# Performance work log

Hardware: AMD Instinct MI355X
Metric: run time of the kernel (lower is better)

The kernel has to match this reference:

```python
import jax, jax.numpy as jnp
import numpy as np

EMBED_DIM = 256
NUM_HEADS = 8
WINDOW = 64
HEAD_DIM = EMBED_DIM // NUM_HEADS


def setup_inputs() -> dict:
    key = jax.random.key(0)
    k_x, k_w, k_ow = jax.random.split(key, 3)
    B, S, E = 2, 4096, EMBED_DIM
    x = jax.random.normal(k_x, (B, S, E), dtype=jnp.float32)
    # nn.MultiheadAttention params: packed in_proj (q,k,v) and out_proj
    bound = 1.0 / np.sqrt(E)
    in_proj_w = jax.random.uniform(k_w, (3 * E, E), jnp.float32, -bound, bound)
    in_proj_b = jnp.zeros((3 * E,), jnp.float32)
    out_w = jax.random.uniform(k_ow, (E, E), jnp.float32, -bound, bound)
    out_b = jnp.zeros((E,), jnp.float32)
    return {"x": x, "in_proj_w": in_proj_w, "in_proj_b": in_proj_b,
            "out_w": out_w, "out_b": out_b}


def reference(x, in_proj_w, in_proj_b, out_w, out_b):
    B, S, E = x.shape
    H, D = NUM_HEADS, HEAD_DIM
    # packed qkv projection (torch Linear: y = x @ W^T + b)
    qkv = jnp.einsum('bse,fe->bsf', x, in_proj_w) + in_proj_b  # [B,S,3E]
    q, k, v = jnp.split(qkv, 3, axis=-1)
    q = q.reshape(B, S, H, D).transpose(0, 2, 1, 3)  # [B,H,S,D]
    k = k.reshape(B, S, H, D).transpose(0, 2, 1, 3)
    v = v.reshape(B, S, H, D).transpose(0, 2, 1, 3)
    scale = 1.0 / jnp.sqrt(jnp.asarray(D, x.dtype))
    scores = jnp.einsum('bhqd,bhkd->bhqk', q * scale, k)  # [B,H,S,S]
    idx = jnp.arange(S)
    band = jnp.abs(idx[:, None] - idx[None, :]) <= WINDOW  # [S,S]
    neg = jnp.asarray(-1e9, scores.dtype)
    scores = jnp.where(band[None, None, :, :], scores, neg)
    attn = jax.nn.softmax(scores, axis=-1)
    out = jnp.einsum('bhqk,bhkd->bhqd', attn, v)  # [B,H,S,D]
    out = out.transpose(0, 2, 1, 3).reshape(B, S, E)
    return jnp.einsum('bse,fe->bsf', out, out_w) + out_b
```

## Files before the change

### kernel.cpp

```cpp
#include <hip/hip_runtime.h>
#include <hip/hip_bf16.h>

#define S_LEN 4096
#define EMB   256
#define NHEAD 8
#define HDIM  32
#define WIN   64
#define BATCH 2

typedef __attribute__((ext_vector_type(8))) short short8;
typedef __attribute__((ext_vector_type(4))) float floatx4;

static __device__ __forceinline__ unsigned int bf16_rn(float x) {
    unsigned int u = __float_as_uint(x);
    return (u + 0x7FFFu + ((u >> 16) & 1u)) >> 16;
}
static __device__ __forceinline__ void split2(float x, unsigned int& hi, unsigned int& lo) {
    hi = bf16_rn(x);
    const float hf = __uint_as_float(hi << 16);
    lo = bf16_rn(x - hf);
}
static __device__ __forceinline__ void split_store4(unsigned short* hp, unsigned short* lp, float4 v) {
    unsigned int h0, l0, h1, l1, h2, l2, h3, l3;
    split2(v.x, h0, l0); split2(v.y, h1, l1);
    split2(v.z, h2, l2); split2(v.w, h3, l3);
    uint2 hv, lv;
    hv.x = h0 | (h1 << 16); hv.y = h2 | (h3 << 16);
    lv.x = l0 | (l1 << 16); lv.y = l2 | (l3 << 16);
    *(uint2*)hp = hv;
    *(uint2*)lp = lv;
}

#define LDA 40

__global__ __launch_bounds__(256) void qkv_proj_kernel(
    const float* __restrict__ X, const float* __restrict__ W,
    const float* __restrict__ bias,
    float* __restrict__ Qb, float* __restrict__ Kb, float* __restrict__ Vb)
{
    __shared__ __align__(16) unsigned short Ah[128 * LDA], Al[128 * LDA];
    __shared__ __align__(16) unsigned short Bh[64 * LDA],  Bl[64 * LDA];
    const int tid = threadIdx.x;
    const int m0 = blockIdx.y * 128, n0 = blockIdx.x * 64;
    const int r0 = tid >> 3, c4 = tid & 7;
    const int lane = tid & 63, wv = tid >> 6;
    const int wm = (wv >> 1) * 64, wn = (wv & 1) * 32;
    const int lm = lane & 15, kq = lane >> 4;

    float4 ar[4], wr[2];
#pragma unroll
    for (int r = 0; r < 4; ++r)
        ar[r] = *(const float4*)(X + (size_t)(m0 + r0 + r * 32) * EMB + c4 * 4);
#pragma unroll
    for (int r = 0; r < 2; ++r)
        wr[r] = *(const float4*)(W + (size_t)(n0 + r0 + r * 32) * EMB + c4 * 4);

    floatx4 acc[4][2] = {};
    for (int t = 0; t < 8; ++t) {
        __syncthreads();
#pragma unroll
        for (int r = 0; r < 4; ++r)
            split_store4(&Ah[(r0 + r * 32) * LDA + c4 * 4], &Al[(r0 + r * 32) * LDA + c4 * 4], ar[r]);
#pragma unroll
        for (int r = 0; r < 2; ++r)
            split_store4(&Bh[(r0 + r * 32) * LDA + c4 * 4], &Bl[(r0 + r * 32) * LDA + c4 * 4], wr[r]);
        __syncthreads();
        if (t < 7) {
            const int k0 = (t + 1) * 32;
#pragma unroll
            for (int r = 0; r < 4; ++r)
                ar[r] = *(const float4*)(X + (size_t)(m0 + r0 + r * 32) * EMB + k0 + c4 * 4);
#pragma unroll
            for (int r = 0; r < 2; ++r)
                wr[r] = *(const float4*)(W + (size_t)(n0 + r0 + r * 32) * EMB + k0 + c4 * 4);
        }
        short8 a_h[4], a_l[4], b_h[2], b_l[2];
#pragma unroll
        for (int mt = 0; mt < 4; ++mt) {
            a_h[mt] = *(const short8*)&Ah[(wm + mt * 16 + lm) * LDA + kq * 8];
            a_l[mt] = *(const short8*)&Al[(wm + mt * 16 + lm) * LDA + kq * 8];
        }
#pragma unroll
        for (int nt = 0; nt < 2; ++nt) {
            b_h[nt] = *(const short8*)&Bh[(wn + nt * 16 + lm) * LDA + kq * 8];
            b_l[nt] = *(const short8*)&Bl[(wn + nt * 16 + lm) * LDA + kq * 8];
        }
#pragma unroll
        for (int mt = 0; mt < 4; ++mt)
#pragma unroll
            for (int nt = 0; nt < 2; ++nt) {
                acc[mt][nt] = __builtin_amdgcn_mfma_f32_16x16x32_bf16(a_h[mt], b_h[nt], acc[mt][nt], 0, 0, 0);
                acc[mt][nt] = __builtin_amdgcn_mfma_f32_16x16x32_bf16(a_h[mt], b_l[nt], acc[mt][nt], 0, 0, 0);
                acc[mt][nt] = __builtin_amdgcn_mfma_f32_16x16x32_bf16(a_l[mt], b_h[nt], acc[mt][nt], 0, 0, 0);
            }
    }
#pragma unroll
    for (int nt = 0; nt < 2; ++nt) {
        const int f = n0 + wn + nt * 16 + lm;
        const int which = f >> 8;
        const int h = (f & 255) >> 5, d = f & 31;
        float* dst = (which == 0) ? Qb : ((which == 1) ? Kb : Vb);
        const float sc = (which == 0) ? 0.17677669529663687f : 1.0f;
        const float bf = bias[f];
#pragma unroll
        for (int mt = 0; mt < 4; ++mt)
#pragma unroll
            for (int r = 0; r < 4; ++r) {
                const int m = m0 + wm + mt * 16 + kq * 4 + r;
                const int b = m >> 12, s = m & (S_LEN - 1);
                dst[(((size_t)b * NHEAD + h) * S_LEN + s) * HDIM + d] = (acc[mt][nt][r] + bf) * sc;
            }
    }
}

__global__ __launch_bounds__(256) void out_proj_kernel(
    const float* __restrict__ A, const float* __restrict__ W,
    const float* __restrict__ bias, float* __restrict__ C)
{
    __shared__ __align__(16) unsigned short Ah[128 * LDA], Al[128 * LDA];
    __shared__ __align__(16) unsigned short Bh[64 * LDA],  Bl[64 * LDA];
    const int tid = threadIdx.x;
    const int m0 = blockIdx.y * 128, n0 = blockIdx.x * 64;
    const int r0 = tid >> 3, c4 = tid & 7;
    const int lane = tid & 63, wv = tid >> 6;
    const int wm = (wv >> 1) * 64, wn = (wv & 1) * 32;
    const int lm = lane & 15, kq = lane >> 4;

    float4 ar[4], wr[2];
#pragma unroll
    for (int r = 0; r < 4; ++r)
        ar[r] = *(const float4*)(A + (size_t)(m0 + r0 + r * 32) * EMB + c4 * 4);
#pragma unroll
    for (int r = 0; r < 2; ++r)
        wr[r] = *(const float4*)(W + (size_t)(n0 + r0 + r * 32) * EMB + c4 * 4);

    floatx4 acc[4][2] = {};
    for (int t = 0; t < 8; ++t) {
        __syncthreads();
#pragma unroll
        for (int r = 0; r < 4; ++r)
            split_store4(&Ah[(r0 + r * 32) * LDA + c4 * 4], &Al[(r0 + r * 32) * LDA + c4 * 4], ar[r]);
#pragma unroll
        for (int r = 0; r < 2; ++r)
            split_store4(&Bh[(r0 + r * 32) * LDA + c4 * 4], &Bl[(r0 + r * 32) * LDA + c4 * 4], wr[r]);
        __syncthreads();
        if (t < 7) {
            const int k0 = (t + 1) * 32;
#pragma unroll
            for (int r = 0; r < 4; ++r)
                ar[r] = *(const float4*)(A + (size_t)(m0 + r0 + r * 32) * EMB + k0 + c4 * 4);
#pragma unroll
            for (int r = 0; r < 2; ++r)
                wr[r] = *(const float4*)(W + (size_t)(n0 + r0 + r * 32) * EMB + k0 + c4 * 4);
        }
        short8 a_h[4], a_l[4], b_h[2], b_l[2];
#pragma unroll
        for (int mt = 0; mt < 4; ++mt) {
            a_h[mt] = *(const short8*)&Ah[(wm + mt * 16 + lm) * LDA + kq * 8];
            a_l[mt] = *(const short8*)&Al[(wm + mt * 16 + lm) * LDA + kq * 8];
        }
#pragma unroll
        for (int nt = 0; nt < 2; ++nt) {
            b_h[nt] = *(const short8*)&Bh[(wn + nt * 16 + lm) * LDA + kq * 8];
            b_l[nt] = *(const short8*)&Bl[(wn + nt * 16 + lm) * LDA + kq * 8];
        }
#pragma unroll
        for (int mt = 0; mt < 4; ++mt)
#pragma unroll
            for (int nt = 0; nt < 2; ++nt) {
                acc[mt][nt] = __builtin_amdgcn_mfma_f32_16x16x32_bf16(a_h[mt], b_h[nt], acc[mt][nt], 0, 0, 0);
                acc[mt][nt] = __builtin_amdgcn_mfma_f32_16x16x32_bf16(a_h[mt], b_l[nt], acc[mt][nt], 0, 0, 0);
                acc[mt][nt] = __builtin_amdgcn_mfma_f32_16x16x32_bf16(a_l[mt], b_h[nt], acc[mt][nt], 0, 0, 0);
            }
    }
#pragma unroll
    for (int nt = 0; nt < 2; ++nt) {
        const int f = n0 + wn + nt * 16 + lm;
        const float bf = bias[f];
#pragma unroll
        for (int mt = 0; mt < 4; ++mt)
#pragma unroll
            for (int r = 0; r < 4; ++r) {
                const int m = m0 + wm + mt * 16 + kq * 4 + r;
                C[(size_t)m * EMB + f] = acc[mt][nt][r] + bf;
            }
    }
}

#define AKS 40
#define AVS 200
#define APS 200

__global__ __launch_bounds__(256) void local_attn_kernel(
    const float* __restrict__ Qb, const float* __restrict__ Kb,
    const float* __restrict__ Vb, float* __restrict__ Ab)
{
    __shared__ __align__(16) unsigned short Qh[64 * AKS], Ql[64 * AKS];
    __shared__ __align__(16) unsigned short Kh[192 * AKS], Kl[192 * AKS];
    __shared__ __align__(16) unsigned short Vt[32 * AVS];
    __shared__ __align__(16) unsigned short Pw[4 * 16 * APS];

    const int tid = threadIdx.x;
    const int q0 = blockIdx.x * 64;
    const int h = blockIdx.y, b = blockIdx.z;
    const int jmin = max(0, q0 - WIN);
    const int jmax = min(S_LEN - 1, q0 + 63 + WIN);
    const int nk = jmax - jmin + 1;
    const size_t bhS = ((size_t)b * NHEAD + h) * S_LEN;
    const float* Qg = Qb + (bhS + q0) * HDIM;
    const float* Kg = Kb + (bhS + jmin) * HDIM;
    const float* Vg = Vb + (bhS + jmin) * HDIM;

    const int r0 = tid >> 3, c4 = tid & 7;
#pragma unroll
    for (int r = 0; r < 2; ++r) {
        const int row = r0 + r * 32;
        const float4 v = *(const float4*)&Qg[row * HDIM + c4 * 4];
        split_store4(&Qh[row * AKS + c4 * 4], &Ql[row * AKS + c4 * 4], v);
    }
#pragma unroll
    for (int r = 0; r < 6; ++r) {
        const int t = r0 + r * 32;
        const int tc = min(t, nk - 1);
        const float4 v = *(const float4*)&Kg[tc * HDIM + c4 * 4];
        split_store4(&Kh[t * AKS + c4 * 4], &Kl[t * AKS + c4 * 4], v);
    }
#pragma unroll
    for (int r = 0; r < 6; ++r) {
        const int t = r0 + r * 32;
        const int tc = min(t, nk - 1);
        const float4 v = *(const float4*)&Vg[tc * HDIM + c4 * 4];
        Vt[(c4 * 4 + 0) * AVS + t] = (unsigned short)bf16_rn(v.x);
        Vt[(c4 * 4 + 1) * AVS + t] = (unsigned short)bf16_rn(v.y);
        Vt[(c4 * 4 + 2) * AVS + t] = (unsigned short)bf16_rn(v.z);
        Vt[(c4 * 4 + 3) * AVS + t] = (unsigned short)bf16_rn(v.w);
    }
    __syncthreads();

    const int lane = tid & 63, wv = tid >> 6;
    const int lm = lane & 15, quad = lane >> 4;
    const int qbase = wv * 16;

    const short8 qh = *(const short8*)&Qh[(qbase + lm) * AKS + quad * 8];
    const short8 ql = *(const short8*)&Ql[(qbase + lm) * AKS + quad * 8];

    floatx4 sacc[12];
#pragma unroll
    for (int nt = 0; nt < 12; ++nt) {
        const short8 bh = *(const short8*)&Kh[(nt * 16 + lm) * AKS + quad * 8];
        const short8 bl = *(const short8*)&Kl[(nt * 16 + lm) * AKS + quad * 8];
        floatx4 a = {};
        a = __builtin_amdgcn_mfma_f32_16x16x32_bf16(qh, bh, a, 0, 0, 0);
        a = __builtin_amdgcn_mfma_f32_16x16x32_bf16(qh, bl, a, 0, 0, 0);
        a = __builtin_amdgcn_mfma_f32_16x16x32_bf16(ql, bh, a, 0, 0, 0);
        sacc[nt] = a;
    }

    const int qg = q0 + qbase + quad * 4;
    float mx[4] = {-1e30f, -1e30f, -1e30f, -1e30f};
#pragma unroll
    for (int nt = 0; nt < 12; ++nt) {
        const int slot = nt * 16 + lm;
        const int keyg = jmin + slot;
#pragma unroll
        for (int r = 0; r < 4; ++r) {
            const int qr = qg + r;
            const bool valid = (slot < nk) && (keyg >= qr - WIN) && (keyg <= qr + WIN);
            const float sv = valid ? sacc[nt][r] : -1e30f;
            sacc[nt][r] = sv;
            mx[r] = fmaxf(mx[r], sv);
        }
    }
#pragma unroll
    for (int r = 0; r < 4; ++r) {
        mx[r] = fmaxf(mx[r], __shfl_xor(mx[r], 1));
        mx[r] = fmaxf(mx[r], __shfl_xor(mx[r], 2));
        mx[r] = fmaxf(mx[r], __shfl_xor(mx[r], 4));
        mx[r] = fmaxf(mx[r], __shfl_xor(mx[r], 8));
    }
    float l[4] = {0.f, 0.f, 0.f, 0.f};
    unsigned short* Pme = &Pw[wv * 16 * APS];
#pragma unroll
    for (int nt = 0; nt < 12; ++nt)
#pragma unroll
        for (int r = 0; r < 4; ++r) {
            const float p = __expf(sacc[nt][r] - mx[r]);
            l[r] += p;
            Pme[(quad * 4 + r) * APS + nt * 16 + lm] = (unsigned short)bf16_rn(p);
        }
#pragma unroll
    for (int r = 0; r < 4; ++r) {
        l[r] += __shfl_xor(l[r], 1);
        l[r] += __shfl_xor(l[r], 2);
        l[r] += __shfl_xor(l[r], 4);
        l[r] += __shfl_xor(l[r], 8);
    }
    const float rl[4] = {1.f / l[0], 1.f / l[1], 1.f / l[2], 1.f / l[3]};

    floatx4 oacc[2] = {};
#pragma unroll
    for (int ks = 0; ks < 6; ++ks) {
        const short8 ap  = *(const short8*)&Pme[lm * APS + ks * 32 + quad * 8];
        const short8 bv0 = *(const short8*)&Vt[lm * AVS + ks * 32 + quad * 8];
        const short8 bv1 = *(const short8*)&Vt[(16 + lm) * AVS + ks * 32 + quad * 8];
        oacc[0] = __builtin_amdgcn_mfma_f32_16x16x32_bf16(ap, bv0, oacc[0], 0, 0, 0);
        oacc[1] = __builtin_amdgcn_mfma_f32_16x16x32_bf16(ap, bv1, oacc[1], 0, 0, 0);
    }
#pragma unroll
    for (int nt = 0; nt < 2; ++nt)
#pragma unroll
        for (int r = 0; r < 4; ++r) {
            const int qrow = qbase + quad * 4 + r;
            Ab[((size_t)b * S_LEN + q0 + qrow) * EMB + h * HDIM + nt * 16 + lm]
                = oacc[nt][r] * rl[r];
        }
}

extern "C" void kernel_launch(void* const* d_in, const int* in_sizes, int n_in,
                              void* d_out, int out_size, void* d_ws, size_t ws_size,
                              hipStream_t stream) {
    const float* x  = (const float*)d_in[0];
    const float* wi = (const float*)d_in[1];
    const float* bi = (const float*)d_in[2];
    const float* wo = (const float*)d_in[3];
    const float* bo = (const float*)d_in[4];
    float* out = (float*)d_out;

    const size_t per = (size_t)BATCH * NHEAD * S_LEN * HDIM;
    float* Qb = (float*)d_ws;
    float* Kb = Qb + per;
    float* Vb = Kb + per;
    float* Ab = Vb + per;

    qkv_proj_kernel<<<dim3(768 / 64, 8192 / 128), 256, 0, stream>>>(x, wi, bi, Qb, Kb, Vb);
    local_attn_kernel<<<dim3(S_LEN / 64, NHEAD, BATCH), 256, 0, stream>>>(Qb, Kb, Vb, Ab);
    out_proj_kernel<<<dim3(256 / 64, 8192 / 128), 256, 0, stream>>>(Ab, wo, bo, out);
}
```

Baseline: 117.0 us.

## Pre-split inputs into bf16 hi/lo once and pass bf16 intermediates between kernels

Adds a conversion kernel that splits X and both weight matrices into bf16 hi/lo planes once, instead of every GEMM block re-splitting fp32 tiles. Q/K/V and the attention output are now stored as bf16 hi/lo (V as a single bf16), so the GEMM and attention kernels load pre-split data with straight 16-byte copies into shared memory. This removes redundant split arithmetic across the 12 column blocks of the QKV GEMM and replaces fp32 intermediates with two bf16 planes. In exchange it adds an extra launch and a full pass over X, and the scalar 2-byte epilogue stores may be poorly coalesced.

```diff
diff --git a/kernel.cpp b/kernel.cpp
--- a/kernel.cpp
+++ b/kernel.cpp
@@ -10,6 +10,7 @@
 
 typedef __attribute__((ext_vector_type(8))) short short8;
 typedef __attribute__((ext_vector_type(4))) float floatx4;
+typedef unsigned short u16;
 
 static __device__ __forceinline__ unsigned int bf16_rn(float x) {
     unsigned int u = __float_as_uint(x);
@@ -20,7 +21,7 @@
     const float hf = __uint_as_float(hi << 16);
     lo = bf16_rn(x - hf);
 }
-static __device__ __forceinline__ void split_store4(unsigned short* hp, unsigned short* lp, float4 v) {
+static __device__ __forceinline__ void split_store4(u16* hp, u16* lp, float4 v) {
     unsigned int h0, l0, h1, l1, h2, l2, h3, l3;
     split2(v.x, h0, l0); split2(v.y, h1, l1);
     split2(v.z, h2, l2); split2(v.w, h3, l3);
@@ -31,48 +32,72 @@
     *(uint2*)lp = lv;
 }
 
+#define NX4 524288
+#define NW4 49152
+#define NO4 16384
+
+__global__ __launch_bounds__(256) void convert_kernel(
+    const float* __restrict__ X, const float* __restrict__ Wi, const float* __restrict__ Wo,
+    u16* __restrict__ Xh, u16* __restrict__ Xl,
+    u16* __restrict__ Wih, u16* __restrict__ Wil,
+    u16* __restrict__ Woh, u16* __restrict__ Wol)
+{
+    const int i = blockIdx.x * 256 + threadIdx.x;
+    const float* src; u16 *dh, *dl; int off;
+    if (i < NX4)            { src = X;  dh = Xh;  dl = Xl;  off = i; }
+    else if (i < NX4 + NW4) { src = Wi; dh = Wih; dl = Wil; off = i - NX4; }
+    else                    { src = Wo; dh = Woh; dl = Wol; off = i - NX4 - NW4; }
+    const float4 v = *(const float4*)(src + (size_t)off * 4);
+    split_store4(dh + (size_t)off * 4, dl + (size_t)off * 4, v);
+}
+
 #define LDA 40
 
 __global__ __launch_bounds__(256) void qkv_proj_kernel(
-    const float* __restrict__ X, const float* __restrict__ W,
+    const u16* __restrict__ Xh, const u16* __restrict__ Xl,
+    const u16* __restrict__ Wh, const u16* __restrict__ Wl,
     const float* __restrict__ bias,
-    float* __restrict__ Qb, float* __restrict__ Kb, float* __restrict__ Vb)
+    u16* __restrict__ Qh, u16* __restrict__ Ql,
+    u16* __restrict__ Kh, u16* __restrict__ Kl, u16* __restrict__ Vb)
 {
-    __shared__ __align__(16) unsigned short Ah[128 * LDA], Al[128 * LDA];
-    __shared__ __align__(16) unsigned short Bh[64 * LDA],  Bl[64 * LDA];
+    __shared__ __align__(16) u16 Ah[128 * LDA], Al[128 * LDA];
+    __shared__ __align__(16) u16 Bh[64 * LDA],  Bl[64 * LDA];
     const int tid = threadIdx.x;
     const int m0 = blockIdx.y * 128, n0 = blockIdx.x * 64;
-    const int r0 = tid >> 3, c4 = tid & 7;
+    const int srow = tid >> 2, sc = tid & 3;
     const int lane = tid & 63, wv = tid >> 6;
     const int wm = (wv >> 1) * 64, wn = (wv & 1) * 32;
     const int lm = lane & 15, kq = lane >> 4;
 
-    float4 ar[4], wr[2];
-#pragma unroll
-    for (int r = 0; r < 4; ++r)
-        ar[r] = *(const float4*)(X + (size_t)(m0 + r0 + r * 32) * EMB + c4 * 4);
-#pragma unroll
-    for (int r = 0; r < 2; ++r)
-        wr[r] = *(const float4*)(W + (size_t)(n0 + r0 + r * 32) * EMB + c4 * 4);
+    uint4 pah[2], pal[2], pbh, pbl;
+#pragma unroll
+    for (int r = 0; r < 2; ++r) {
+        pah[r] = *(const uint4*)(Xh + (size_t)(m0 + srow + r * 64) * EMB + sc * 8);
+        pal[r] = *(const uint4*)(Xl + (size_t)(m0 + srow + r * 64) * EMB + sc * 8);
+    }
+    pbh = *(const uint4*)(Wh + (size_t)(n0 + srow) * EMB + sc * 8);
+    pbl = *(const uint4*)(Wl + (size_t)(n0 + srow) * EMB + sc * 8);
 
     floatx4 acc[4][2] = {};
     for (int t = 0; t < 8; ++t) {
         __syncthreads();
 #pragma unroll
-        for (int r = 0; r < 4; ++r)
-            split_store4(&Ah[(r0 + r * 32) * LDA + c4 * 4], &Al[(r0 + r * 32) * LDA + c4 * 4], ar[r]);
-#pragma unroll
-        for (int r = 0; r < 2; ++r)
-            split_store4(&Bh[(r0 + r * 32) * LDA + c4 * 4], &Bl[(r0 + r * 32) * LDA + c4 * 4], wr[r]);
+        for (int r = 0; r < 2; ++r) {
+            *(uint4*)&Ah[(srow + r * 64) * LDA + sc * 8] = pah[r];
+            *(uint4*)&Al[(srow + r * 64) * LDA + sc * 8] = pal[r];
+        }
+        *(uint4*)&Bh[srow * LDA + sc * 8] = pbh;
+        *(uint4*)&Bl[srow * LDA + sc * 8] = pbl;
         __syncthreads();
         if (t < 7) {
             const int k0 = (t + 1) * 32;
 #pragma unroll
-            for (int r = 0; r < 4; ++r)
-                ar[r] = *(const float4*)(X + (size_t)(m0 + r0 + r * 32) * EMB + k0 + c4 * 4);
-#pragma unroll
-            for (int r = 0; r < 2; ++r)
-                wr[r] = *(const float4*)(W + (size_t)(n0 + r0 + r * 32) * EMB + k0 + c4 * 4);
+            for (int r = 0; r < 2; ++r) {
+                pah[r] = *(const uint4*)(Xh + (size_t)(m0 + srow + r * 64) * EMB + k0 + sc * 8);
+                pal[r] = *(const uint4*)(Xl + (size_t)(m0 + srow + r * 64) * EMB + k0 + sc * 8);
+            }
+            pbh = *(const uint4*)(Wh + (size_t)(n0 + srow) * EMB + k0 + sc * 8);
+            pbl = *(const uint4*)(Wl + (size_t)(n0 + srow) * EMB + k0 + sc * 8);
         }
         short8 a_h[4], a_l[4], b_h[2], b_l[2];
 #pragma unroll
@@ -99,8 +124,7 @@
         const int f = n0 + wn + nt * 16 + lm;
         const int which = f >> 8;
         const int h = (f & 255) >> 5, d = f & 31;
-        float* dst = (which == 0) ? Qb : ((which == 1) ? Kb : Vb);
-        const float sc = (which == 0) ? 0.17677669529663687f : 1.0f;
+        const float sc2 = (which == 0) ? 0.17677669529663687f : 1.0f;
         const float bf = bias[f];
 #pragma unroll
         for (int mt = 0; mt < 4; ++mt)
@@ -108,50 +132,63 @@
             for (int r = 0; r < 4; ++r) {
                 const int m = m0 + wm + mt * 16 + kq * 4 + r;
                 const int b = m >> 12, s = m & (S_LEN - 1);
-                dst[(((size_t)b * NHEAD + h) * S_LEN + s) * HDIM + d] = (acc[mt][nt][r] + bf) * sc;
+                const float v = (acc[mt][nt][r] + bf) * sc2;
+                const size_t off = (((size_t)b * NHEAD + h) * S_LEN + s) * HDIM + d;
+                if (which == 2) {
+                    Vb[off] = (u16)bf16_rn(v);
+                } else {
+                    unsigned int hi, lo;
+                    split2(v, hi, lo);
+                    if (which == 0) { Qh[off] = (u16)hi; Ql[off] = (u16)lo; }
+                    else            { Kh[off] = (u16)hi; Kl[off] = (u16)lo; }
+                }
             }
     }
 }
 
 __global__ __launch_bounds__(256) void out_proj_kernel(
-    const float* __restrict__ A, const float* __restrict__ W,
+    const u16* __restrict__ Abh, const u16* __restrict__ Abl,
+    const u16* __restrict__ Wh, const u16* __restrict__ Wl,
     const float* __restrict__ bias, float* __restrict__ C)
 {
-    __shared__ __align__(16) unsigned short Ah[128 * LDA], Al[128 * LDA];
-    __shared__ __align__(16) unsigned short Bh[64 * LDA],  Bl[64 * LDA];
+    __shared__ __align__(16) u16 Ah[128 * LDA], Al[128 * LDA];
+    __shared__ __align__(16) u16 Bh[64 * LDA],  Bl[64 * LDA];
     const int tid = threadIdx.x;
     const int m0 = blockIdx.y * 128, n0 = blockIdx.x * 64;
-    const int r0 = tid >> 3, c4 = tid & 7;
+    const int srow = tid >> 2, sc = tid & 3;
     const int lane = tid & 63, wv = tid >> 6;
     const int wm = (wv >> 1) * 64, wn = (wv & 1) * 32;
     const int lm = lane & 15, kq = lane >> 4;
 
-    float4 ar[4], wr[2];
-#pragma unroll
-    for (int r = 0; r < 4; ++r)
-        ar[r] = *(const float4*)(A + (size_t)(m0 + r0 + r * 32) * EMB + c4 * 4);
-#pragma unroll
-    for (int r = 0; r < 2; ++r)
-        wr[r] = *(const float4*)(W + (size_t)(n0 + r0 + r * 32) * EMB + c4 * 4);
+    uint4 pah[2], pal[2], pbh, pbl;
+#pragma unroll
+    for (int r = 0; r < 2; ++r) {
+        pah[r] = *(const uint4*)(Abh + (size_t)(m0 + srow + r * 64) * EMB + sc * 8);
+        pal[r] = *(const uint4*)(Abl + (size_t)(m0 + srow + r * 64) * EMB + sc * 8);
+    }
+    pbh = *(const uint4*)(Wh + (size_t)(n0 + srow) * EMB + sc * 8);
+    pbl = *(const uint4*)(Wl + (size_t)(n0 + srow) * EMB + sc * 8);
 
     floatx4 acc[4][2] = {};
     for (int t = 0; t < 8; ++t) {
         __syncthreads();
 #pragma unroll
-        for (int r = 0; r < 4; ++r)
-            split_store4(&Ah[(r0 + r * 32) * LDA + c4 * 4], &Al[(r0 + r * 32) * LDA + c4 * 4], ar[r]);
-#pragma unroll
-        for (int r = 0; r < 2; ++r)
-            split_store4(&Bh[(r0 + r * 32) * LDA + c4 * 4], &Bl[(r0 + r * 32) * LDA + c4 * 4], wr[r]);
+        for (int r = 0; r < 2; ++r) {
+            *(uint4*)&Ah[(srow + r * 64) * LDA + sc * 8] = pah[r];
+            *(uint4*)&Al[(srow + r * 64) * LDA + sc * 8] = pal[r];
+        }
+        *(uint4*)&Bh[srow * LDA + sc * 8] = pbh;
+        *(uint4*)&Bl[srow * LDA + sc * 8] = pbl;
         __syncthreads();
         if (t < 7) {
             const int k0 = (t + 1) * 32;
 #pragma unroll
-            for (int r = 0; r < 4; ++r)
-                ar[r] = *(const float4*)(A + (size_t)(m0 + r0 + r * 32) * EMB + k0 + c4 * 4);
-#pragma unroll
-            for (int r = 0; r < 2; ++r)
-                wr[r] = *(const float4*)(W + (size_t)(n0 + r0 + r * 32) * EMB + k0 + c4 * 4);
+            for (int r = 0; r < 2; ++r) {
+                pah[r] = *(const uint4*)(Abh + (size_t)(m0 + srow + r * 64) * EMB + k0 + sc * 8);
+                pal[r] = *(const uint4*)(Abl + (size_t)(m0 + srow + r * 64) * EMB + k0 + sc * 8);
+            }
+            pbh = *(const uint4*)(Wh + (size_t)(n0 + srow) * EMB + k0 + sc * 8);
+            pbl = *(const uint4*)(Wl + (size_t)(n0 + srow) * EMB + k0 + sc * 8);
         }
         short8 a_h[4], a_l[4], b_h[2], b_l[2];
 #pragma unroll
@@ -192,13 +229,15 @@
 #define APS 200
 
 __global__ __launch_bounds__(256) void local_attn_kernel(
-    const float* __restrict__ Qb, const float* __restrict__ Kb,
-    const float* __restrict__ Vb, float* __restrict__ Ab)
+    const u16* __restrict__ Qhg, const u16* __restrict__ Qlg,
+    const u16* __restrict__ Khg, const u16* __restrict__ Klg,
+    const u16* __restrict__ Vbg,
+    u16* __restrict__ Abh, u16* __restrict__ Abl)
 {
-    __shared__ __align__(16) unsigned short Qh[64 * AKS], Ql[64 * AKS];
-    __shared__ __align__(16) unsigned short Kh[192 * AKS], Kl[192 * AKS];
-    __shared__ __align__(16) unsigned short Vt[32 * AVS];
-    __shared__ __align__(16) unsigned short Pw[4 * 16 * APS];
+    __shared__ __align__(16) u16 Qh[64 * AKS], Ql[64 * AKS];
+    __shared__ __align__(16) u16 Kh[192 * AKS], Kl[192 * AKS];
+    __shared__ __align__(16) u16 Vt[32 * AVS];
+    __shared__ __align__(16) u16 Pw[4 * 16 * APS];
 
     const int tid = threadIdx.x;
     const int q0 = blockIdx.x * 64;
@@ -207,33 +246,39 @@
     const int jmax = min(S_LEN - 1, q0 + 63 + WIN);
     const int nk = jmax - jmin + 1;
     const size_t bhS = ((size_t)b * NHEAD + h) * S_LEN;
-    const float* Qg = Qb + (bhS + q0) * HDIM;
-    const float* Kg = Kb + (bhS + jmin) * HDIM;
-    const float* Vg = Vb + (bhS + jmin) * HDIM;
-
-    const int r0 = tid >> 3, c4 = tid & 7;
-#pragma unroll
-    for (int r = 0; r < 2; ++r) {
-        const int row = r0 + r * 32;
-        const float4 v = *(const float4*)&Qg[row * HDIM + c4 * 4];
-        split_store4(&Qh[row * AKS + c4 * 4], &Ql[row * AKS + c4 * 4], v);
-    }
-#pragma unroll
-    for (int r = 0; r < 6; ++r) {
-        const int t = r0 + r * 32;
+    const size_t qoff = (bhS + q0) * HDIM;
+    const size_t koff = (bhS + jmin) * HDIM;
+
+    const int srow = tid >> 2, sc = tid & 3;
+    {
+        const uint4 vh = *(const uint4*)(Qhg + qoff + (size_t)srow * HDIM + sc * 8);
+        const uint4 vl = *(const uint4*)(Qlg + qoff + (size_t)srow * HDIM + sc * 8);
+        *(uint4*)&Qh[srow * AKS + sc * 8] = vh;
+        *(uint4*)&Ql[srow * AKS + sc * 8] = vl;
+    }
+#pragma unroll
+    for (int r = 0; r < 3; ++r) {
+        const int t = srow + r * 64;
         const int tc = min(t, nk - 1);
-        const float4 v = *(const float4*)&Kg[tc * HDIM + c4 * 4];
-        split_store4(&Kh[t * AKS + c4 * 4], &Kl[t * AKS + c4 * 4], v);
-    }
-#pragma unroll
-    for (int r = 0; r < 6; ++r) {
-        const int t = r0 + r * 32;
+        const uint4 vh = *(const uint4*)(Khg + koff + (size_t)tc * HDIM + sc * 8);
+        const uint4 vl = *(const uint4*)(Klg + koff + (size_t)tc * HDIM + sc * 8);
+        *(uint4*)&Kh[t * AKS + sc * 8] = vh;
+        *(uint4*)&Kl[t * AKS + sc * 8] = vl;
+    }
+#pragma unroll
+    for (int r = 0; r < 3; ++r) {
+        const int t = srow + r * 64;
         const int tc = min(t, nk - 1);
-        const float4 v = *(const float4*)&Vg[tc * HDIM + c4 * 4];
-        Vt[(c4 * 4 + 0) * AVS + t] = (unsigned short)bf16_rn(v.x);
-        Vt[(c4 * 4 + 1) * AVS + t] = (unsigned short)bf16_rn(v.y);
-        Vt[(c4 * 4 + 2) * AVS + t] = (unsigned short)bf16_rn(v.z);
-        Vt[(c4 * 4 + 3) * AVS + t] = (unsigned short)bf16_rn(v.w);
+        const uint4 v = *(const uint4*)(Vbg + koff + (size_t)tc * HDIM + sc * 8);
+        const int d0 = sc * 8;
+        Vt[(d0 + 0) * AVS + t] = (u16)(v.x & 0xFFFF);
+        Vt[(d0 + 1) * AVS + t] = (u16)(v.x >> 16);
+        Vt[(d0 + 2) * AVS + t] = (u16)(v.y & 0xFFFF);
+        Vt[(d0 + 3) * AVS + t] = (u16)(v.y >> 16);
+        Vt[(d0 + 4) * AVS + t] = (u16)(v.z & 0xFFFF);
+        Vt[(d0 + 5) * AVS + t] = (u16)(v.z >> 16);
+        Vt[(d0 + 6) * AVS + t] = (u16)(v.w & 0xFFFF);
+        Vt[(d0 + 7) * AVS + t] = (u16)(v.w >> 16);
     }
     __syncthreads();
 
@@ -279,14 +324,14 @@
         mx[r] = fmaxf(mx[r], __shfl_xor(mx[r], 8));
     }
     float l[4] = {0.f, 0.f, 0.f, 0.f};
-    unsigned short* Pme = &Pw[wv * 16 * APS];
+    u16* Pme = &Pw[wv * 16 * APS];
 #pragma unroll
     for (int nt = 0; nt < 12; ++nt)
 #pragma unroll
         for (int r = 0; r < 4; ++r) {
             const float p = __expf(sacc[nt][r] - mx[r]);
             l[r] += p;
-            Pme[(quad * 4 + r) * APS + nt * 16 + lm] = (unsigned short)bf16_rn(p);
+            Pme[(quad * 4 + r) * APS + nt * 16 + lm] = (u16)bf16_rn(p);
         }
 #pragma unroll
     for (int r = 0; r < 4; ++r) {
@@ -311,8 +356,12 @@
 #pragma unroll
         for (int r = 0; r < 4; ++r) {
             const int qrow = qbase + quad * 4 + r;
-            Ab[((size_t)b * S_LEN + q0 + qrow) * EMB + h * HDIM + nt * 16 + lm]
-                = oacc[nt][r] * rl[r];
+            const float v = oacc[nt][r] * rl[r];
+            unsigned int hi, lo;
+            split2(v, hi, lo);
+            const size_t off = ((size_t)b * S_LEN + q0 + qrow) * EMB + h * HDIM + nt * 16 + lm;
+            Abh[off] = (u16)hi;
+            Abl[off] = (u16)lo;
         }
 }
 
@@ -327,12 +376,27 @@
     float* out = (float*)d_out;
 
     const size_t per = (size_t)BATCH * NHEAD * S_LEN * HDIM;
-    float* Qb = (float*)d_ws;
-    float* Kb = Qb + per;
-    float* Vb = Kb + per;
-    float* Ab = Vb + per;
-
-    qkv_proj_kernel<<<dim3(768 / 64, 8192 / 128), 256, 0, stream>>>(x, wi, bi, Qb, Kb, Vb);
-    local_attn_kernel<<<dim3(S_LEN / 64, NHEAD, BATCH), 256, 0, stream>>>(Qb, Kb, Vb, Ab);
-    out_proj_kernel<<<dim3(256 / 64, 8192 / 128), 256, 0, stream>>>(Ab, wo, bo, out);
-}
+    u16* p = (u16*)d_ws;
+    u16* Xh  = p; p += per;
+    u16* Xl  = p; p += per;
+    u16* Wih = p; p += 768 * EMB;
+    u16* Wil = p; p += 768 * EMB;
+    u16* Woh = p; p += EMB * EMB;
+    u16* Wol = p; p += EMB * EMB;
+    u16* Qh  = p; p += per;
+    u16* Ql  = p; p += per;
+    u16* Kh  = p; p += per;
+    u16* Kl  = p; p += per;
+    u16* Vb  = p; p += per;
+    u16* Abh = p; p += per;
+    u16* Abl = p; p += per;
+
+    convert_kernel<<<dim3((NX4 + NW4 + NO4) / 256), 256, 0, stream>>>(
+        x, wi, wo, Xh, Xl, Wih, Wil, Woh, Wol);
+    qkv_proj_kernel<<<dim3(768 / 64, 8192 / 128), 256, 0, stream>>>(
+        Xh, Xl, Wih, Wil, bi, Qh, Ql, Kh, Kl, Vb);
+    local_attn_kernel<<<dim3(S_LEN / 64, NHEAD, BATCH), 256, 0, stream>>>(
+        Qh, Ql, Kh, Kl, Vb, Abh, Abl);
+    out_proj_kernel<<<dim3(256 / 64, 8192 / 128), 256, 0, stream>>>(
+        Abh, Abl, Woh, Wol, bo, out);
+}
```

Measured after the change: 142.3 us. +21.7%, slower.
